# Kernel tuning notes

Hardware: AMD Instinct MI355X
Metric: run time of the kernel (lower is better)

Reference implementation:

```python
import jax, jax.numpy as jnp
import numpy as np

N_NODES = 200000
N_EDGES = 6400000
IN_DIM = 15      # pfc_input_dim
POS_DIM = 4      # positional_dim
OUT_DIM = 2      # vtx_classes + 1


def setup_inputs() -> dict:
    key = jax.random.key(0)
    k1, k2, k3, k4, k5, k6, k7 = jax.random.split(key, 7)
    x_pfc = jax.random.normal(k1, (N_NODES, IN_DIM), dtype=jnp.float32)
    edge_index = jax.random.randint(k2, (2, N_EDGES), 0, N_NODES, dtype=jnp.int64)
    s_in = 1.0 / np.sqrt(IN_DIM)
    s_pos = 1.0 / np.sqrt(POS_DIM)
    # PointTransformerConv params: lin, lin_src, lin_dst (no bias), pos_nn = Linear(4, 2)
    W_lin = jax.random.uniform(k3, (OUT_DIM, IN_DIM), jnp.float32, -s_in, s_in)
    W_src = jax.random.uniform(k4, (OUT_DIM, IN_DIM), jnp.float32, -s_in, s_in)
    W_dst = jax.random.uniform(k5, (OUT_DIM, IN_DIM), jnp.float32, -s_in, s_in)
    W_pos = jax.random.uniform(k6, (OUT_DIM, POS_DIM), jnp.float32, -s_pos, s_pos)
    b_pos = jax.random.uniform(k7, (OUT_DIM,), jnp.float32, -s_pos, s_pos)
    return {"x_pfc": x_pfc, "edge_index": edge_index, "W_lin": W_lin,
            "W_src": W_src, "W_dst": W_dst, "W_pos": W_pos, "b_pos": b_pos}


def reference(x_pfc, edge_index, W_lin, W_src, W_dst, W_pos, b_pos):
    n = x_pfc.shape[0]
    pos = x_pfc[:, :POS_DIM]
    # original forward calls ptc_only(x, pos, edge_index.flip(0)):
    # source j = edge_index[1], target i = edge_index[0]
    j = edge_index[1]
    i = edge_index[0]
    # node-level linear maps (N x OUT_DIM)
    v = x_pfc @ W_lin.T
    a_src = x_pfc @ W_src.T
    a_dst = x_pfc @ W_dst.T
    # positional MLP on relative positions (E x OUT_DIM)
    delta = (pos[i] - pos[j]) @ W_pos.T + b_pos
    alpha = a_dst[i] - a_src[j] + delta
    # segment softmax over incoming edges of each target node i
    m = jax.ops.segment_max(alpha, i, num_segments=n)  # -inf for empty segments (never indexed)
    e = jnp.exp(alpha - m[i])
    denom = jax.ops.segment_sum(e, i, num_segments=n)
    attn = e / (denom[i] + 1e-16)
    msg = attn * (v[j] + delta)
    return jax.ops.segment_sum(msg, i, num_segments=n)
```

## Files before the change

kernel.cpp:

```cpp
#include <hip/hip_runtime.h>

#define N_NODES 200000
#define N_EDGES 6400000
#define IN_DIM 15
#define POS_DIM 4

#define CSHIFT 9
#define CMASK 511
#define CW 512
#define NCOARSE ((N_NODES + CW - 1) >> CSHIFT)
#define CHUNK 16384
#define NBLK ((N_EDGES + CHUNK - 1) / CHUNK)
#define CAP 17408

typedef unsigned uv4 __attribute__((ext_vector_type(4)));

__global__ void node_prep(const float* __restrict__ x,
                          const float* __restrict__ Wlin,
                          const float* __restrict__ Wsrc,
                          const float* __restrict__ Wdst,
                          const float* __restrict__ Wpos,
                          float2* __restrict__ tabI,
                          float4* __restrict__ tabJ,
                          float2* __restrict__ pvec)
{
    int n = blockIdx.x * blockDim.x + threadIdx.x;
    if (n >= N_NODES) return;
    const float* xp = x + (long)n * IN_DIM;
    float xv[IN_DIM];
#pragma unroll
    for (int k = 0; k < IN_DIM; ++k) xv[k] = xp[k];

    float p0 = 0.f, p1 = 0.f;
#pragma unroll
    for (int k = 0; k < POS_DIM; ++k) {
        p0 += Wpos[k] * xv[k];
        p1 += Wpos[POS_DIM + k] * xv[k];
    }
    float v0 = 0.f, v1 = 0.f, as0 = 0.f, as1 = 0.f, ad0 = 0.f, ad1 = 0.f;
#pragma unroll
    for (int k = 0; k < IN_DIM; ++k) {
        float xk = xv[k];
        v0  += Wlin[k] * xk;           v1  += Wlin[IN_DIM + k] * xk;
        as0 += Wsrc[k] * xk;           as1 += Wsrc[IN_DIM + k] * xk;
        ad0 += Wdst[k] * xk;           ad1 += Wdst[IN_DIM + k] * xk;
    }
    tabI[n] = make_float2(ad0 + p0, ad1 + p1);
    tabJ[n] = make_float4(as0 + p0, as1 + p1, v0 - p0, v1 - p1);
    pvec[n] = make_float2(p0, p1);
}

__global__ void hist_kernel(const int* __restrict__ idx,
                            unsigned* __restrict__ hist)
{
    __shared__ unsigned h[NCOARSE];
    for (int t = threadIdx.x; t < NCOARSE; t += blockDim.x) h[t] = 0u;
    __syncthreads();
    long s0 = (long)blockIdx.x * CHUNK;
    int end = (int)min((long)CHUNK, (long)N_EDGES - s0);
    for (int t = threadIdx.x * 4; t < end; t += 2048) {
        int4 iv = *(const int4*)(idx + s0 + t);
        atomicAdd(&h[iv.x >> CSHIFT], 1u);
        atomicAdd(&h[iv.y >> CSHIFT], 1u);
        atomicAdd(&h[iv.z >> CSHIFT], 1u);
        atomicAdd(&h[iv.w >> CSHIFT], 1u);
    }
    __syncthreads();
    for (int t = threadIdx.x; t < NCOARSE; t += blockDim.x)
        hist[(unsigned)blockIdx.x * NCOARSE + t] = h[t];
}

__global__ void colscan_kernel(unsigned* __restrict__ hist,
                               unsigned* __restrict__ totals)
{
    __shared__ unsigned s[512];
    int k = blockIdx.x;
    int t = threadIdx.x;
    unsigned v = (t < NBLK) ? hist[(unsigned)t * NCOARSE + k] : 0u;
    s[t] = v;
    __syncthreads();
    for (int off = 1; off < 512; off <<= 1) {
        unsigned add = (t >= off) ? s[t - off] : 0u;
        __syncthreads();
        s[t] += add;
        __syncthreads();
    }
    if (t < NBLK) hist[(unsigned)t * NCOARSE + k] = s[t] - v;
    if (t == NBLK - 1) totals[k] = s[t];
}

__global__ void basescan_kernel(const unsigned* __restrict__ totals,
                                unsigned* __restrict__ base)
{
    __shared__ unsigned s[512];
    int t = threadIdx.x;
    unsigned v = (t < NCOARSE) ? ((totals[t] + 3u) & ~3u) : 0u;
    s[t] = v;
    __syncthreads();
    for (int off = 1; off < 512; off <<= 1) {
        unsigned a = (t >= off) ? s[t - off] : 0u;
        __syncthreads();
        s[t] += a;
        __syncthreads();
    }
    if (t < NCOARSE) base[t] = s[t] - v;
}

__global__ void scatter_kernel(const int* __restrict__ idx,
                               const unsigned* __restrict__ hist,
                               const unsigned* __restrict__ base,
                               unsigned* __restrict__ packed)
{
    __shared__ unsigned stage[CHUNK];
    __shared__ unsigned cnt[512];
    __shared__ unsigned sc[512];
    __shared__ unsigned lloc[512];
    __shared__ unsigned gdst[NCOARSE];
    int b = blockIdx.x;
    int t = threadIdx.x;
    long s0 = (long)b * CHUNK;
    int end = (int)min((long)CHUNK, (long)N_EDGES - s0);
    cnt[t] = 0u;
    __syncthreads();
    for (int e = t * 4; e < end; e += 2048) {
        int4 iv = *(const int4*)(idx + s0 + e);
        atomicAdd(&cnt[iv.x >> CSHIFT], 1u);
        atomicAdd(&cnt[iv.y >> CSHIFT], 1u);
        atomicAdd(&cnt[iv.z >> CSHIFT], 1u);
        atomicAdd(&cnt[iv.w >> CSHIFT], 1u);
    }
    __syncthreads();
    sc[t] = cnt[t];
    __syncthreads();
    for (int o = 1; o < 512; o <<= 1) {
        unsigned a = (t >= o) ? sc[t - o] : 0u;
        __syncthreads();
        sc[t] += a;
        __syncthreads();
    }
    {
        unsigned ex = sc[t] - cnt[t];
        lloc[t] = ex;
        cnt[t] = ex;
        if (t < NCOARSE) gdst[t] = base[t] + hist[(unsigned)b * NCOARSE + t];
    }
    __syncthreads();
    for (int e = t * 4; e < end; e += 2048) {
        int4 iv = *(const int4*)(idx + s0 + e);
        int4 jv = *(const int4*)(idx + N_EDGES + s0 + e);
        unsigned r0 = atomicAdd(&cnt[iv.x >> CSHIFT], 1u);
        unsigned r1 = atomicAdd(&cnt[iv.y >> CSHIFT], 1u);
        unsigned r2 = atomicAdd(&cnt[iv.z >> CSHIFT], 1u);
        unsigned r3 = atomicAdd(&cnt[iv.w >> CSHIFT], 1u);
        stage[r0] = ((unsigned)jv.x << CSHIFT) | (unsigned)(iv.x & CMASK);
        stage[r1] = ((unsigned)jv.y << CSHIFT) | (unsigned)(iv.y & CMASK);
        stage[r2] = ((unsigned)jv.z << CSHIFT) | (unsigned)(iv.z & CMASK);
        stage[r3] = ((unsigned)jv.w << CSHIFT) | (unsigned)(iv.w & CMASK);
    }
    __syncthreads();
    int wid = t >> 6, lane = t & 63;
    for (int bk = wid; bk < NCOARSE; bk += 8) {
        unsigned st = lloc[bk];
        unsigned len = ((bk + 1 < 512) ? lloc[bk + 1] : (unsigned)end) - st;
        unsigned gd = gdst[bk];
        for (unsigned e = lane; e < len; e += 64u)
            packed[gd + e] = stage[st + e];
    }
}

__global__ void bucket_agg_kernel(const unsigned* __restrict__ packed,
                                  const unsigned* __restrict__ base,
                                  const unsigned* __restrict__ totals,
                                  const float2* __restrict__ tabI,
                                  const float4* __restrict__ tabJ,
                                  const float2* __restrict__ pvec,
                                  const float* __restrict__ bpos,
                                  float2* __restrict__ out)
{
    __shared__ unsigned cache[CAP + 512];
    __shared__ unsigned cnt[512], sc[512], cur[512];
    int k = blockIdx.x;
    int t = threadIdx.x;
    unsigned s = base[k];
    unsigned n = min(totals[k], (unsigned)CAP);
    cnt[t] = 0u;
    __syncthreads();
    for (unsigned e = 4u * t; e < n; e += 2048u) {
        uv4 p = *(const uv4*)(packed + s + e);
        atomicAdd(&cnt[p.x & CMASK], 1u);
        if (e + 1 < n) atomicAdd(&cnt[p.y & CMASK], 1u);
        if (e + 2 < n) atomicAdd(&cnt[p.z & CMASK], 1u);
        if (e + 3 < n) atomicAdd(&cnt[p.w & CMASK], 1u);
    }
    __syncthreads();
    sc[t] = cnt[t];
    __syncthreads();
    for (int o = 1; o < 512; o <<= 1) {
        unsigned a = (t >= o) ? sc[t - o] : 0u;
        __syncthreads();
        sc[t] += a;
        __syncthreads();
    }
    unsigned deg = cnt[t];
    unsigned st  = sc[t] - deg + (unsigned)t;
    cur[t] = st;
    __syncthreads();
    for (unsigned e = 4u * t; e < n; e += 2048u) {
        uv4 p = __builtin_nontemporal_load((const uv4*)(packed + s + e));
        { unsigned pos = atomicAdd(&cur[p.x & CMASK], 1u); cache[pos] = p.x >> CSHIFT; }
        if (e + 1 < n) { unsigned pos = atomicAdd(&cur[p.y & CMASK], 1u); cache[pos] = p.y >> CSHIFT; }
        if (e + 2 < n) { unsigned pos = atomicAdd(&cur[p.z & CMASK], 1u); cache[pos] = p.z >> CSHIFT; }
        if (e + 3 < n) { unsigned pos = atomicAdd(&cur[p.w & CMASK], 1u); cache[pos] = p.w >> CSHIFT; }
    }
    __syncthreads();
    float b0 = bpos[0], b1 = bpos[1];
    int gn = (k << CSHIFT) + t;
    if (gn >= N_NODES) return;
    float2 fi = tabI[gn];
    float a0 = fi.x + b0, a1 = fi.y + b1;
    float sn0 = 0.f, sn1 = 0.f, sd0 = 0.f, sd1 = 0.f;
    unsigned e = 0;
    for (; e + 4u <= deg; e += 4u) {
        unsigned j0 = cache[st + e],     j1 = cache[st + e + 1];
        unsigned j2 = cache[st + e + 2], j3 = cache[st + e + 3];
        float4 f0 = tabJ[j0], f1 = tabJ[j1], f2 = tabJ[j2], f3 = tabJ[j3];
        float e00 = __expf(a0 - f0.x), e01 = __expf(a1 - f0.y);
        float e10 = __expf(a0 - f1.x), e11 = __expf(a1 - f1.y);
        float e20 = __expf(a0 - f2.x), e21 = __expf(a1 - f2.y);
        float e30 = __expf(a0 - f3.x), e31 = __expf(a1 - f3.y);
        sn0 += e00 * f0.z + e10 * f1.z + e20 * f2.z + e30 * f3.z;
        sn1 += e01 * f0.w + e11 * f1.w + e21 * f2.w + e31 * f3.w;
        sd0 += e00 + e10 + e20 + e30;
        sd1 += e01 + e11 + e21 + e31;
    }
    for (; e < deg; ++e) {
        unsigned j = cache[st + e];
        float4 fj = tabJ[j];
        float e0 = __expf(a0 - fj.x), e1 = __expf(a1 - fj.y);
        sn0 += e0 * fj.z;  sn1 += e1 * fj.w;
        sd0 += e0;         sd1 += e1;
    }
    float2 p = pvec[gn];
    float o0 = (sn0 + (p.x + b0) * sd0) / (sd0 + 1e-16f);
    float o1 = (sn1 + (p.y + b1) * sd1) / (sd1 + 1e-16f);
    out[gn] = make_float2(o0, o1);
}

extern "C" void kernel_launch(void* const* d_in, const int* in_sizes, int n_in,
                              void* d_out, int out_size, void* d_ws, size_t ws_size,
                              hipStream_t stream) {
    const float* x    = (const float*)d_in[0];
    const int*   idx  = (const int*)d_in[1];
    const float* Wlin = (const float*)d_in[2];
    const float* Wsrc = (const float*)d_in[3];
    const float* Wdst = (const float*)d_in[4];
    const float* Wpos = (const float*)d_in[5];
    const float* bpos = (const float*)d_in[6];
    float* out = (float*)d_out;

    char* ws = (char*)d_ws;
    size_t off = 0;
    float4* tabJ = (float4*)(ws + off); off += (size_t)N_NODES * 16;
    float2* tabI = (float2*)(ws + off); off += (size_t)N_NODES * 8;
    float2* pvec = (float2*)(ws + off); off += (size_t)N_NODES * 8;
    unsigned* packed = (unsigned*)(ws + off); off += ((size_t)N_EDGES + 4u * NCOARSE) * 4;
    unsigned* hist   = (unsigned*)(ws + off); off += (size_t)NBLK * NCOARSE * 4;
    unsigned* totals = (unsigned*)(ws + off); off += (size_t)NCOARSE * 4;
    unsigned* base   = (unsigned*)(ws + off); off += (size_t)NCOARSE * 4;

    node_prep<<<(N_NODES + 255) / 256, 256, 0, stream>>>(x, Wlin, Wsrc, Wdst, Wpos,
                                                         tabI, tabJ, pvec);
    hist_kernel<<<NBLK, 512, 0, stream>>>(idx, hist);
    colscan_kernel<<<NCOARSE, 512, 0, stream>>>(hist, totals);
    basescan_kernel<<<1, 512, 0, stream>>>(totals, base);
    scatter_kernel<<<NBLK, 512, 0, stream>>>(idx, hist, base, packed);
    bucket_agg_kernel<<<NCOARSE, 512, 0, stream>>>(packed, base, totals,
                                                   tabI, tabJ, pvec, bpos,
                                                   (float2*)out);
}
```

Measured before the change: 175.5 us.

## Drop histogram/scan passes; use fixed-capacity buckets and LDS float atomics for aggregation

Removes the hist, column-scan and base-scan kernels. Buckets now have fixed CAP-sized slots, and each scatter block claims its output offset with a global atomicAdd on a per-bucket counter that node_prep zeroes. The aggregation kernel skips the in-LDS counting sort by target: each edge accumulates its exp terms directly into per-target LDS accumulators with workgroup-scope float atomics, and the destination-side linear terms are recomputed from x in place of the tabI/pvec tables. This cuts three launches and several passes over the edge list, at the cost of heavy LDS atomic contention and a non-deterministic float summation order.

```diff
diff --git a/kernel.cpp b/kernel.cpp
--- a/kernel.cpp
+++ b/kernel.cpp
@@ -15,16 +15,19 @@
 
 typedef unsigned uv4 __attribute__((ext_vector_type(4)));
 
+__device__ __forceinline__ void lds_fadd(float* p, float v) {
+    (void)__hip_atomic_fetch_add(p, v, __ATOMIC_RELAXED, __HIP_MEMORY_SCOPE_WORKGROUP);
+}
+
 __global__ void node_prep(const float* __restrict__ x,
                           const float* __restrict__ Wlin,
                           const float* __restrict__ Wsrc,
-                          const float* __restrict__ Wdst,
                           const float* __restrict__ Wpos,
-                          float2* __restrict__ tabI,
                           float4* __restrict__ tabJ,
-                          float2* __restrict__ pvec)
+                          unsigned* __restrict__ gcnt)
 {
     int n = blockIdx.x * blockDim.x + threadIdx.x;
+    if (n < NCOARSE) gcnt[n] = 0u;
     if (n >= N_NODES) return;
     const float* xp = x + (long)n * IN_DIM;
     float xv[IN_DIM];
@@ -37,78 +40,18 @@
         p0 += Wpos[k] * xv[k];
         p1 += Wpos[POS_DIM + k] * xv[k];
     }
-    float v0 = 0.f, v1 = 0.f, as0 = 0.f, as1 = 0.f, ad0 = 0.f, ad1 = 0.f;
+    float v0 = 0.f, v1 = 0.f, as0 = 0.f, as1 = 0.f;
 #pragma unroll
     for (int k = 0; k < IN_DIM; ++k) {
         float xk = xv[k];
-        v0  += Wlin[k] * xk;           v1  += Wlin[IN_DIM + k] * xk;
-        as0 += Wsrc[k] * xk;           as1 += Wsrc[IN_DIM + k] * xk;
-        ad0 += Wdst[k] * xk;           ad1 += Wdst[IN_DIM + k] * xk;
-    }
-    tabI[n] = make_float2(ad0 + p0, ad1 + p1);
+        v0  += Wlin[k] * xk;  v1  += Wlin[IN_DIM + k] * xk;
+        as0 += Wsrc[k] * xk;  as1 += Wsrc[IN_DIM + k] * xk;
+    }
     tabJ[n] = make_float4(as0 + p0, as1 + p1, v0 - p0, v1 - p1);
-    pvec[n] = make_float2(p0, p1);
-}
-
-__global__ void hist_kernel(const int* __restrict__ idx,
-                            unsigned* __restrict__ hist)
-{
-    __shared__ unsigned h[NCOARSE];
-    for (int t = threadIdx.x; t < NCOARSE; t += blockDim.x) h[t] = 0u;
-    __syncthreads();
-    long s0 = (long)blockIdx.x * CHUNK;
-    int end = (int)min((long)CHUNK, (long)N_EDGES - s0);
-    for (int t = threadIdx.x * 4; t < end; t += 2048) {
-        int4 iv = *(const int4*)(idx + s0 + t);
-        atomicAdd(&h[iv.x >> CSHIFT], 1u);
-        atomicAdd(&h[iv.y >> CSHIFT], 1u);
-        atomicAdd(&h[iv.z >> CSHIFT], 1u);
-        atomicAdd(&h[iv.w >> CSHIFT], 1u);
-    }
-    __syncthreads();
-    for (int t = threadIdx.x; t < NCOARSE; t += blockDim.x)
-        hist[(unsigned)blockIdx.x * NCOARSE + t] = h[t];
-}
-
-__global__ void colscan_kernel(unsigned* __restrict__ hist,
-                               unsigned* __restrict__ totals)
-{
-    __shared__ unsigned s[512];
-    int k = blockIdx.x;
-    int t = threadIdx.x;
-    unsigned v = (t < NBLK) ? hist[(unsigned)t * NCOARSE + k] : 0u;
-    s[t] = v;
-    __syncthreads();
-    for (int off = 1; off < 512; off <<= 1) {
-        unsigned add = (t >= off) ? s[t - off] : 0u;
-        __syncthreads();
-        s[t] += add;
-        __syncthreads();
-    }
-    if (t < NBLK) hist[(unsigned)t * NCOARSE + k] = s[t] - v;
-    if (t == NBLK - 1) totals[k] = s[t];
-}
-
-__global__ void basescan_kernel(const unsigned* __restrict__ totals,
-                                unsigned* __restrict__ base)
-{
-    __shared__ unsigned s[512];
-    int t = threadIdx.x;
-    unsigned v = (t < NCOARSE) ? ((totals[t] + 3u) & ~3u) : 0u;
-    s[t] = v;
-    __syncthreads();
-    for (int off = 1; off < 512; off <<= 1) {
-        unsigned a = (t >= off) ? s[t - off] : 0u;
-        __syncthreads();
-        s[t] += a;
-        __syncthreads();
-    }
-    if (t < NCOARSE) base[t] = s[t] - v;
 }
 
 __global__ void scatter_kernel(const int* __restrict__ idx,
-                               const unsigned* __restrict__ hist,
-                               const unsigned* __restrict__ base,
+                               unsigned* __restrict__ gcnt,
                                unsigned* __restrict__ packed)
 {
     __shared__ unsigned stage[CHUNK];
@@ -139,10 +82,11 @@
         __syncthreads();
     }
     {
-        unsigned ex = sc[t] - cnt[t];
+        unsigned c  = cnt[t];
+        unsigned ex = sc[t] - c;
         lloc[t] = ex;
+        if (t < NCOARSE) gdst[t] = atomicAdd(&gcnt[t], c);
         cnt[t] = ex;
-        if (t < NCOARSE) gdst[t] = base[t] + hist[(unsigned)b * NCOARSE + t];
     }
     __syncthreads();
     for (int e = t * 4; e < end; e += 2048) {
@@ -160,89 +104,111 @@
     __syncthreads();
     int wid = t >> 6, lane = t & 63;
     for (int bk = wid; bk < NCOARSE; bk += 8) {
-        unsigned st = lloc[bk];
-        unsigned len = ((bk + 1 < 512) ? lloc[bk + 1] : (unsigned)end) - st;
-        unsigned gd = gdst[bk];
+        unsigned st  = lloc[bk];
+        unsigned len = lloc[bk + 1] - st;
+        unsigned gb  = gdst[bk];
+        unsigned rem = (gb < (unsigned)CAP) ? (unsigned)CAP - gb : 0u;
+        if (len > rem) len = rem;
+        unsigned* dst = packed + (size_t)bk * CAP + gb;
         for (unsigned e = lane; e < len; e += 64u)
-            packed[gd + e] = stage[st + e];
-    }
-}
-
-__global__ void bucket_agg_kernel(const unsigned* __restrict__ packed,
-                                  const unsigned* __restrict__ base,
-                                  const unsigned* __restrict__ totals,
-                                  const float2* __restrict__ tabI,
-                                  const float4* __restrict__ tabJ,
-                                  const float2* __restrict__ pvec,
-                                  const float* __restrict__ bpos,
-                                  float2* __restrict__ out)
-{
-    __shared__ unsigned cache[CAP + 512];
-    __shared__ unsigned cnt[512], sc[512], cur[512];
+            dst[e] = stage[st + e];
+    }
+}
+
+
+struct AggState {
+    float2* als;
+    float (*acc)[4];
+};
+
+__device__ __forceinline__ void edge_one(unsigned w, const float2* als,
+                                         float (*acc)[4],
+                                         const float4* __restrict__ tabJ)
+{
+    unsigned r = w & CMASK;
+    float4 fj = tabJ[w >> CSHIFT];
+    float2 a = als[r];
+    float e0 = __expf(a.x - fj.x), e1 = __expf(a.y - fj.y);
+    lds_fadd(&acc[r][0], e0);
+    lds_fadd(&acc[r][1], e1);
+    lds_fadd(&acc[r][2], e0 * fj.z);
+    lds_fadd(&acc[r][3], e1 * fj.w);
+}
+
+__global__ __launch_bounds__(512) void
+bucket_agg_kernel(const unsigned* __restrict__ packed,
+                  const unsigned* __restrict__ gcnt,
+                  const float* __restrict__ x,
+                  const float* __restrict__ Wdst,
+                  const float* __restrict__ Wpos,
+                  const float4* __restrict__ tabJ,
+                  const float* __restrict__ bpos,
+                  float2* __restrict__ out)
+{
+    __shared__ float2 als[512];
+    __shared__ float  acc[512][4];
     int k = blockIdx.x;
     int t = threadIdx.x;
-    unsigned s = base[k];
-    unsigned n = min(totals[k], (unsigned)CAP);
-    cnt[t] = 0u;
-    __syncthreads();
-    for (unsigned e = 4u * t; e < n; e += 2048u) {
-        uv4 p = *(const uv4*)(packed + s + e);
-        atomicAdd(&cnt[p.x & CMASK], 1u);
-        if (e + 1 < n) atomicAdd(&cnt[p.y & CMASK], 1u);
-        if (e + 2 < n) atomicAdd(&cnt[p.z & CMASK], 1u);
-        if (e + 3 < n) atomicAdd(&cnt[p.w & CMASK], 1u);
-    }
-    __syncthreads();
-    sc[t] = cnt[t];
-    __syncthreads();
-    for (int o = 1; o < 512; o <<= 1) {
-        unsigned a = (t >= o) ? sc[t - o] : 0u;
-        __syncthreads();
-        sc[t] += a;
-        __syncthreads();
-    }
-    unsigned deg = cnt[t];
-    unsigned st  = sc[t] - deg + (unsigned)t;
-    cur[t] = st;
-    __syncthreads();
-    for (unsigned e = 4u * t; e < n; e += 2048u) {
-        uv4 p = __builtin_nontemporal_load((const uv4*)(packed + s + e));
-        { unsigned pos = atomicAdd(&cur[p.x & CMASK], 1u); cache[pos] = p.x >> CSHIFT; }
-        if (e + 1 < n) { unsigned pos = atomicAdd(&cur[p.y & CMASK], 1u); cache[pos] = p.y >> CSHIFT; }
-        if (e + 2 < n) { unsigned pos = atomicAdd(&cur[p.z & CMASK], 1u); cache[pos] = p.z >> CSHIFT; }
-        if (e + 3 < n) { unsigned pos = atomicAdd(&cur[p.w & CMASK], 1u); cache[pos] = p.w >> CSHIFT; }
-    }
-    __syncthreads();
     float b0 = bpos[0], b1 = bpos[1];
     int gn = (k << CSHIFT) + t;
+
+    float p0 = 0.f, p1 = 0.f, ad0 = 0.f, ad1 = 0.f;
+    if (gn < N_NODES) {
+        const float* xp = x + (long)gn * IN_DIM;
+        float xv[IN_DIM];
+#pragma unroll
+        for (int q = 0; q < IN_DIM; ++q) xv[q] = xp[q];
+#pragma unroll
+        for (int q = 0; q < POS_DIM; ++q) {
+            p0 += Wpos[q] * xv[q];
+            p1 += Wpos[POS_DIM + q] * xv[q];
+        }
+#pragma unroll
+        for (int q = 0; q < IN_DIM; ++q) {
+            ad0 += Wdst[q] * xv[q];
+            ad1 += Wdst[IN_DIM + q] * xv[q];
+        }
+    }
+    als[t] = make_float2(ad0 + p0 + b0, ad1 + p1 + b1);
+    acc[t][0] = 0.f; acc[t][1] = 0.f; acc[t][2] = 0.f; acc[t][3] = 0.f;
+    __syncthreads();
+
+    unsigned n = min(gcnt[k], (unsigned)CAP);
+    const unsigned* pk = packed + (size_t)k * CAP;
+
+    for (unsigned e = 4u * t; e < n; e += 2048u) {
+        uv4 p = __builtin_nontemporal_load((const uv4*)(pk + e));
+        if (e + 4u <= n) {
+            unsigned r0 = p.x & CMASK, r1 = p.y & CMASK, r2 = p.z & CMASK, r3 = p.w & CMASK;
+            float4 f0 = tabJ[p.x >> CSHIFT];
+            float4 f1 = tabJ[p.y >> CSHIFT];
+            float4 f2 = tabJ[p.z >> CSHIFT];
+            float4 f3 = tabJ[p.w >> CSHIFT];
+            float2 a0 = als[r0], a1 = als[r1], a2 = als[r2], a3 = als[r3];
+            float e00 = __expf(a0.x - f0.x), e01 = __expf(a0.y - f0.y);
+            float e10 = __expf(a1.x - f1.x), e11 = __expf(a1.y - f1.y);
+            float e20 = __expf(a2.x - f2.x), e21 = __expf(a2.y - f2.y);
+            float e30 = __expf(a3.x - f3.x), e31 = __expf(a3.y - f3.y);
+            lds_fadd(&acc[r0][0], e00);        lds_fadd(&acc[r0][1], e01);
+            lds_fadd(&acc[r0][2], e00 * f0.z); lds_fadd(&acc[r0][3], e01 * f0.w);
+            lds_fadd(&acc[r1][0], e10);        lds_fadd(&acc[r1][1], e11);
+            lds_fadd(&acc[r1][2], e10 * f1.z); lds_fadd(&acc[r1][3], e11 * f1.w);
+            lds_fadd(&acc[r2][0], e20);        lds_fadd(&acc[r2][1], e21);
+            lds_fadd(&acc[r2][2], e20 * f2.z); lds_fadd(&acc[r2][3], e21 * f2.w);
+            lds_fadd(&acc[r3][0], e30);        lds_fadd(&acc[r3][1], e31);
+            lds_fadd(&acc[r3][2], e30 * f3.z); lds_fadd(&acc[r3][3], e31 * f3.w);
+        } else {
+            edge_one(p.x, als, acc, tabJ);
+            if (e + 1u < n) edge_one(p.y, als, acc, tabJ);
+            if (e + 2u < n) edge_one(p.z, als, acc, tabJ);
+        }
+    }
+    __syncthreads();
+
     if (gn >= N_NODES) return;
-    float2 fi = tabI[gn];
-    float a0 = fi.x + b0, a1 = fi.y + b1;
-    float sn0 = 0.f, sn1 = 0.f, sd0 = 0.f, sd1 = 0.f;
-    unsigned e = 0;
-    for (; e + 4u <= deg; e += 4u) {
-        unsigned j0 = cache[st + e],     j1 = cache[st + e + 1];
-        unsigned j2 = cache[st + e + 2], j3 = cache[st + e + 3];
-        float4 f0 = tabJ[j0], f1 = tabJ[j1], f2 = tabJ[j2], f3 = tabJ[j3];
-        float e00 = __expf(a0 - f0.x), e01 = __expf(a1 - f0.y);
-        float e10 = __expf(a0 - f1.x), e11 = __expf(a1 - f1.y);
-        float e20 = __expf(a0 - f2.x), e21 = __expf(a1 - f2.y);
-        float e30 = __expf(a0 - f3.x), e31 = __expf(a1 - f3.y);
-        sn0 += e00 * f0.z + e10 * f1.z + e20 * f2.z + e30 * f3.z;
-        sn1 += e01 * f0.w + e11 * f1.w + e21 * f2.w + e31 * f3.w;
-        sd0 += e00 + e10 + e20 + e30;
-        sd1 += e01 + e11 + e21 + e31;
-    }
-    for (; e < deg; ++e) {
-        unsigned j = cache[st + e];
-        float4 fj = tabJ[j];
-        float e0 = __expf(a0 - fj.x), e1 = __expf(a1 - fj.y);
-        sn0 += e0 * fj.z;  sn1 += e1 * fj.w;
-        sd0 += e0;         sd1 += e1;
-    }
-    float2 p = pvec[gn];
-    float o0 = (sn0 + (p.x + b0) * sd0) / (sd0 + 1e-16f);
-    float o1 = (sn1 + (p.y + b1) * sd1) / (sd1 + 1e-16f);
+    float sd0 = acc[t][0], sd1 = acc[t][1], sn0 = acc[t][2], sn1 = acc[t][3];
+    float o0 = (sn0 + (p0 + b0) * sd0) / (sd0 + 1e-16f);
+    float o1 = (sn1 + (p1 + b1) * sd1) / (sd1 + 1e-16f);
     out[gn] = make_float2(o0, o1);
 }
 
@@ -261,20 +227,13 @@
     char* ws = (char*)d_ws;
     size_t off = 0;
     float4* tabJ = (float4*)(ws + off); off += (size_t)N_NODES * 16;
-    float2* tabI = (float2*)(ws + off); off += (size_t)N_NODES * 8;
-    float2* pvec = (float2*)(ws + off); off += (size_t)N_NODES * 8;
-    unsigned* packed = (unsigned*)(ws + off); off += ((size_t)N_EDGES + 4u * NCOARSE) * 4;
-    unsigned* hist   = (unsigned*)(ws + off); off += (size_t)NBLK * NCOARSE * 4;
-    unsigned* totals = (unsigned*)(ws + off); off += (size_t)NCOARSE * 4;
-    unsigned* base   = (unsigned*)(ws + off); off += (size_t)NCOARSE * 4;
-
-    node_prep<<<(N_NODES + 255) / 256, 256, 0, stream>>>(x, Wlin, Wsrc, Wdst, Wpos,
-                                                         tabI, tabJ, pvec);
-    hist_kernel<<<NBLK, 512, 0, stream>>>(idx, hist);
-    colscan_kernel<<<NCOARSE, 512, 0, stream>>>(hist, totals);
-    basescan_kernel<<<1, 512, 0, stream>>>(totals, base);
-    scatter_kernel<<<NBLK, 512, 0, stream>>>(idx, hist, base, packed);
-    bucket_agg_kernel<<<NCOARSE, 512, 0, stream>>>(packed, base, totals,
-                                                   tabI, tabJ, pvec, bpos,
+    unsigned* packed = (unsigned*)(ws + off); off += (size_t)NCOARSE * CAP * 4;
+    unsigned* gcnt   = (unsigned*)(ws + off); off += (size_t)NCOARSE * 4;
+
+    node_prep<<<(N_NODES + 255) / 256, 256, 0, stream>>>(x, Wlin, Wsrc, Wpos,
+                                                         tabJ, gcnt);
+    scatter_kernel<<<NBLK, 512, 0, stream>>>(idx, gcnt, packed);
+    bucket_agg_kernel<<<NCOARSE, 512, 0, stream>>>(packed, gcnt,
+                                                   x, Wdst, Wpos, tabJ, bpos,
                                                    (float2*)out);
 }
```

Result: slower. 297.7 us (+69.6%).
